# Kernel optimization log

Hardware: AMD Instinct MI355X
Metric: run time of the kernel (lower is better)

Reference implementation:

```python
import jax, jax.numpy as jnp
import numpy as np

N_PER_G = 100  # nodes per graph


def setup_inputs() -> dict:
    key = jax.random.key(0)
    ks = jax.random.split(key, 12)
    N, G, E = 100000, 1000, 1600000
    ninp, nout, K, H, H2 = 3, 10, 5, 64, 32
    x = jax.random.normal(ks[0], (N, ninp), jnp.float32)
    # within-graph random edges (contiguous node blocks per graph)
    epg = E // G
    gid = jnp.arange(E, dtype=jnp.int32) // epg
    src = jax.random.randint(ks[1], (E,), 0, N_PER_G, jnp.int32) + gid * N_PER_G
    dst = jax.random.randint(ks[2], (E,), 0, N_PER_G, jnp.int32) + gid * N_PER_G
    edge_index = jnp.stack([src, dst])
    batch = (jnp.arange(N, dtype=jnp.int32) // N_PER_G)
    lambda_max = 1.5 + 0.5 * jax.random.uniform(ks[3], (G,), jnp.float32)
    s = 0.05
    W1 = jax.random.normal(ks[4], (K, ninp, H), jnp.float32) * s
    b1 = jnp.zeros((H,), jnp.float32)
    W2 = jax.random.normal(ks[5], (K, H, H), jnp.float32) * s
    b2 = jnp.zeros((H,), jnp.float32)
    W3 = jax.random.normal(ks[6], (K, H, H), jnp.float32) * s
    b3 = jnp.zeros((H,), jnp.float32)
    bn_gamma = jnp.ones((H,), jnp.float32)
    bn_beta = jnp.zeros((H,), jnp.float32)
    bn_mean = jnp.zeros((H,), jnp.float32)
    bn_var = jnp.ones((H,), jnp.float32)
    fc1_w = jax.random.normal(ks[7], (H, H2), jnp.float32) * s
    fc1_b = jnp.zeros((H2,), jnp.float32)
    fc2_w = jax.random.normal(ks[8], (H2, nout), jnp.float32) * s
    fc2_b = jnp.zeros((nout,), jnp.float32)
    return dict(x=x, edge_index=edge_index, batch=batch, lambda_max=lambda_max,
                W1=W1, b1=b1, W2=W2, b2=b2, W3=W3, b3=b3,
                bn_gamma=bn_gamma, bn_beta=bn_beta, bn_mean=bn_mean, bn_var=bn_var,
                fc1_w=fc1_w, fc1_b=fc1_b, fc2_w=fc2_w, fc2_b=fc2_b)


def _cheb_conv(x, W, b, row, col, coef_edge, coef_loop):
    # PyG ChebConv with sym-normalized scaled Laplacian:
    # Lhat x = scatter_add(coef_edge * x[col] -> row) + coef_loop * x
    N = x.shape[0]
    def lhat(h):
        return jax.ops.segment_sum(coef_edge[:, None] * h[col], row,
                                   num_segments=N) + coef_loop[:, None] * h
    Tx0 = x
    out = Tx0 @ W[0]
    Tx1 = lhat(x)
    out = out + Tx1 @ W[1]
    for k in range(2, W.shape[0]):
        Tx2 = 2.0 * lhat(Tx1) - Tx0
        out = out + Tx2 @ W[k]
        Tx0, Tx1 = Tx1, Tx2
    return out + b


def reference(x, edge_index, batch, lambda_max,
              W1, b1, W2, b2, W3, b3,
              bn_gamma, bn_beta, bn_mean, bn_var,
              fc1_w, fc1_b, fc2_w, fc2_b):
    N = x.shape[0]
    G = lambda_max.shape[0]
    row, col = edge_index[0], edge_index[1]
    # sym Laplacian normalization, scaled by 2/lambda_max (per-graph)
    deg = jax.ops.segment_sum(jnp.ones_like(row, dtype=x.dtype), row, num_segments=N)
    dis = jnp.where(deg > 0, deg, 1.0) ** -0.5
    dis = jnp.where(deg > 0, dis, 0.0)
    lmax_e = lambda_max[batch[row]]
    coef_edge = -(2.0 / lmax_e) * dis[row] * dis[col]   # off-diagonal of Lhat
    coef_loop = 2.0 / lambda_max[batch] - 1.0           # diagonal of Lhat
    h = jax.nn.relu(_cheb_conv(x, W1, b1, row, col, coef_edge, coef_loop))
    h = jax.nn.relu(_cheb_conv(h, W2, b2, row, col, coef_edge, coef_loop))
    h = jax.nn.relu(_cheb_conv(h, W3, b3, row, col, coef_edge, coef_loop))
    # global mean pool over graphs
    sums = jax.ops.segment_sum(h, batch, num_segments=G)
    cnts = jax.ops.segment_sum(jnp.ones((N,), h.dtype), batch, num_segments=G)
    g = sums / jnp.maximum(cnts, 1.0)[:, None]
    # BatchNorm1d (eval mode, running stats), eps=1e-5
    g = (g - bn_mean) * jax.lax.rsqrt(bn_var + 1e-5) * bn_gamma + bn_beta
    g = jax.nn.relu(g @ fc1_w + fc1_b)
    return jax.nn.log_softmax(g @ fc2_w + fc2_b, axis=1)
```

## Files before the change

kernel.cpp:

```cpp
#include <hip/hip_runtime.h>

#define NPG 100
#define HF 64
#define NROW 128
#define SA 120
#define ST 72
#define CMW 28

typedef float  f4   __attribute__((ext_vector_type(4)));
typedef float  f16v __attribute__((ext_vector_type(16)));
typedef short  bf8  __attribute__((ext_vector_type(8)));

#define SZ_ARM (NROW * SA * 2)
#define SZ_T   (NROW * ST * 2)
#define OFF_ARM 0
#define OFF_T   SZ_ARM
#define OFF_CM  SZ_ARM
#define OFF_MISC (OFF_T + SZ_T)
#define SMEM_BYTES (OFF_MISC + 1280)

#define WT_TOTAL 46080

__device__ __forceinline__ unsigned short f2bf(float f) {
    unsigned u = __float_as_uint(f);
    u += 0x7fffu + ((u >> 16) & 1u);
    return (unsigned short)(u >> 16);
}
__device__ __forceinline__ float bf2f(unsigned short h) {
    return __uint_as_float(((unsigned)h) << 16);
}
__device__ __forceinline__ f16v zerov16() {
    f16v z;
    #pragma unroll
    for (int i = 0; i < 16; i++) z[i] = 0.f;
    return z;
}

__global__ void wconv(const float* __restrict__ W1, const float* __restrict__ W2,
                      const float* __restrict__ W3, unsigned short* __restrict__ ws)
{
    int idx = blockIdx.x * 256 + threadIdx.x;
    if (idx >= WT_TOTAL) return;
    float v;
    if (idx < 5120) {
        int k5 = idx >> 10, rem = idx & 1023, fo = rem >> 4, fi = rem & 15;
        v = (fi < 3) ? W1[(k5 * 3 + fi) * HF + fo] : 0.f;
    } else if (idx < 25600) {
        int j = idx - 5120;
        int k5 = j >> 12, rem = j & 4095, fo = rem >> 6, fi = rem & 63;
        v = W2[(k5 * HF + fi) * HF + fo];
    } else {
        int j = idx - 25600;
        int k5 = j >> 12, rem = j & 4095, fo = rem >> 6, fi = rem & 63;
        v = W3[(k5 * HF + fi) * HF + fo];
    }
    ws[idx] = f2bf(v);
}

__launch_bounds__(256, 2)
__global__ void cheb1b(const float* __restrict__ x, const int* __restrict__ ei,
                       const float* __restrict__ lambda_max,
                       const unsigned short* __restrict__ Wt,
                       const float* __restrict__ b1, const float* __restrict__ b2,
                       const float* __restrict__ b3,
                       const float* __restrict__ bng, const float* __restrict__ bnb,
                       const float* __restrict__ bnm, const float* __restrict__ bnv,
                       const float* __restrict__ fc1w, const float* __restrict__ fc1b,
                       const float* __restrict__ fc2w, const float* __restrict__ fc2b,
                       float* __restrict__ out, int E_total, int epg)
{
    extern __shared__ char sm[];
    const int tid = threadIdx.x;
    const int g = blockIdx.x;
    const int ebase = g * epg, nbase = g * NPG;
    const int wg = tid >> 6, lane = tid & 63;
    const int l31 = lane & 31, hh = lane >> 5;
    const int ht  = wg & 1;
    const int Mt0 = (wg >> 1) * 2;
    const int fo  = ht * 32 + l31;

    unsigned* Cm  = (unsigned*)(sm + OFF_CM);
    float* dis    = (float*)(sm + OFF_MISC);
    float* pool   = (float*)(sm + OFF_MISC + 448);
    float* gvn    = (float*)(sm + OFF_MISC + 704);
    float* zf     = (float*)(sm + OFF_MISC + 960);
    float* logits = (float*)(sm + OFF_MISC + 1088);
    float* lsep   = (float*)(sm + OFF_MISC + 1152);

    const float lam = lambda_max[g];
    const float two_l = 2.0f / lam;
    const float cl = two_l - 1.0f;

    for (int i = tid; i < (NROW * CMW) / 4; i += 256)
        ((f4*)Cm)[i] = (f4){0.f, 0.f, 0.f, 0.f};
    __syncthreads();
    for (int e = tid; e < epg; e += 256) {
        int r = ei[ebase + e] - nbase;
        int c = ei[E_total + ebase + e] - nbase;
        atomicAdd(&Cm[r * CMW + (c >> 2)], 1u << (8 * (c & 3)));
    }
    __syncthreads();
    if (tid < NPG) {
        unsigned s = 0;
        #pragma unroll
        for (int w = 0; w < CMW; w++) {
            unsigned u = Cm[tid * CMW + w];
            s += (u & 255) + ((u >> 8) & 255) + ((u >> 16) & 255) + (u >> 24);
        }
        dis[tid] = s > 0 ? rsqrtf((float)s) : 0.f;
    }
    __syncthreads();
    for (int u = tid; u < NROW * 56; u += 256) {
        int n = u / 56, p = (u % 56) * 2;
        float v0 = 0.f, v1 = 0.f;
        if (n < NPG) {
            unsigned w = Cm[n * CMW + (p >> 2)];
            int sh = 8 * (p & 3);
            float c0 = (float)((w >> sh) & 255);
            float c1 = (float)((w >> (sh + 8)) & 255);
            float base = -two_l * dis[n];
            v0 = (p     < NPG) ? c0 * base * dis[p]     : 0.f;
            v1 = (p + 1 < NPG) ? c1 * base * dis[p + 1] : 0.f;
            if (p == n)     v0 += cl;
            if (p + 1 == n) v1 += cl;
        }
        *(unsigned*)(sm + OFF_ARM + (n * SA + p) * 2) =
            (unsigned)f2bf(v0) | ((unsigned)f2bf(v1) << 16);
    }
    __syncthreads();

    for (int i = tid; i < SZ_T / 16; i += 256)
        ((f4*)(sm + OFF_T))[i] = (f4){0.f, 0.f, 0.f, 0.f};
    if (tid < HF) pool[tid] = 0.f;
    __syncthreads();
    if (tid < NPG) {
        unsigned short h0 = f2bf(x[(nbase + tid) * 3 + 0]);
        unsigned short h1 = f2bf(x[(nbase + tid) * 3 + 1]);
        unsigned short h2 = f2bf(x[(nbase + tid) * 3 + 2]);
        *(unsigned*)(sm + OFF_T + (tid * ST) * 2) = (unsigned)h0 | ((unsigned)h1 << 16);
        *(unsigned short*)(sm + OFF_T + (tid * ST + 2) * 2) = h2;
    }
    __syncthreads();

    f16v acc[2];
    unsigned prev[2][8], oldr[2][8];
    const float* bsv[3] = {b1, b2, b3};

    for (int L = 0; L < 3; L++) {
        const bool l1 = (L == 0);
        const unsigned short* Wl = l1 ? Wt : (Wt + (L == 1 ? 5120 : 25600));
        acc[0] = zerov16();
        acc[1] = zerov16();

        #pragma unroll
        for (int m = 0; m < 2; m++) {
            unsigned short tv[16];
            #pragma unroll
            for (int r = 0; r < 16; r++) {
                int np = (Mt0 + m) * 32 + (r & 3) + 8 * (r >> 2) + 4 * hh;
                tv[r] = *(const unsigned short*)(sm + OFF_T + (np * ST + fo) * 2);
            }
            #pragma unroll
            for (int p = 0; p < 8; p++)
                prev[m][p] = (unsigned)tv[2 * p] | ((unsigned)tv[2 * p + 1] << 16);
        }

        auto TW = [&](int k5) {
            const int nKs = l1 ? 1 : 4;
            for (int Ks = 0; Ks < nKs; Ks++) {
                bf8 bw;
                if (l1) bw = *(const bf8*)(Wl + (k5 * 64 + fo) * 16 + 8 * hh);
                else    bw = *(const bf8*)(Wl + (k5 * 64 + fo) * 64 + Ks * 16 + 8 * hh);
                #pragma unroll
                for (int m = 0; m < 2; m++) {
                    bf8 a = *(const bf8*)(sm + OFF_T +
                              (((Mt0 + m) * 32 + l31) * ST + Ks * 16 + 8 * hh) * 2);
                    acc[m] = __builtin_amdgcn_mfma_f32_32x32x16_bf16(a, bw, acc[m], 0, 0, 0);
                }
            }
        };

        TW(0);
        for (int s = 1; s <= 4; s++) {
            bf8 bfr[7];
            #pragma unroll
            for (int Ks = 0; Ks < 7; Ks++) {
                #pragma unroll
                for (int j = 0; j < 8; j++) {
                    int k = Ks * 16 + 8 * hh + j;
                    bfr[Ks][j] = *(const short*)(sm + OFF_T + (k * ST + fo) * 2);
                }
            }
            __syncthreads();
            #pragma unroll
            for (int m = 0; m < 2; m++) {
                f16v c = zerov16();
                #pragma unroll
                for (int Ks = 0; Ks < 7; Ks++) {
                    bf8 a = *(const bf8*)(sm + OFF_ARM +
                              (((Mt0 + m) * 32 + l31) * SA + Ks * 16 + 8 * hh) * 2);
                    c = __builtin_amdgcn_mfma_f32_32x32x16_bf16(a, bfr[Ks], c, 0, 0, 0);
                }
                unsigned short h[16];
                #pragma unroll
                for (int r = 0; r < 16; r++) {
                    float v = c[r];
                    if (s >= 2) {
                        unsigned short o = (unsigned short)
                            ((oldr[m][r >> 1] >> (16 * (r & 1))) & 0xffff);
                        v = 2.f * v - bf2f(o);
                    }
                    h[r] = f2bf(v);
                }
                #pragma unroll
                for (int p = 0; p < 8; p++) {
                    oldr[m][p] = prev[m][p];
                    prev[m][p] = (unsigned)h[2 * p] | ((unsigned)h[2 * p + 1] << 16);
                }
                #pragma unroll
                for (int r = 0; r < 16; r++) {
                    int np = (Mt0 + m) * 32 + (r & 3) + 8 * (r >> 2) + 4 * hh;
                    *(unsigned short*)(sm + OFF_T + (np * ST + fo) * 2) = h[r];
                }
            }
            __syncthreads();
            TW(s);
        }
        __syncthreads();

        const float bias = bsv[L][fo];
        if (L < 2) {
            #pragma unroll
            for (int m = 0; m < 2; m++) {
                #pragma unroll
                for (int r = 0; r < 16; r++) {
                    float h = fmaxf(acc[m][r] + bias, 0.f);
                    int np = (Mt0 + m) * 32 + (r & 3) + 8 * (r >> 2) + 4 * hh;
                    *(unsigned short*)(sm + OFF_T + (np * ST + fo) * 2) = f2bf(h);
                }
            }
            __syncthreads();
        } else {
            float ssum = 0.f;
            #pragma unroll
            for (int m = 0; m < 2; m++) {
                #pragma unroll
                for (int r = 0; r < 16; r++) {
                    int np = (Mt0 + m) * 32 + (r & 3) + 8 * (r >> 2) + 4 * hh;
                    float h = fmaxf(acc[m][r] + bias, 0.f);
                    if (np < NPG) ssum += h;
                }
            }
            ssum += __shfl_xor(ssum, 32, 64);
            if (hh == 0) atomicAdd(&pool[fo], ssum);
            __syncthreads();
        }
    }

    if (tid < HF) {
        float gv = pool[tid] * (1.0f / NPG);
        gv = (gv - bnm[tid]) * rsqrtf(bnv[tid] + 1e-5f) * bng[tid] + bnb[tid];
        gvn[tid] = gv;
    }
    __syncthreads();
    if (tid < 32) {
        float a = fc1b[tid];
        for (int f = 0; f < HF; f++) a += gvn[f] * fc1w[f * 32 + tid];
        zf[tid] = fmaxf(a, 0.f);
    }
    __syncthreads();
    if (tid < 10) {
        float a = fc2b[tid];
        for (int k = 0; k < 32; k++) a += zf[k] * fc2w[k * 10 + tid];
        logits[tid] = a;
    }
    __syncthreads();
    if (tid == 0) {
        float m = logits[0];
        for (int i = 1; i < 10; i++) m = fmaxf(m, logits[i]);
        float s = 0.f;
        for (int i = 0; i < 10; i++) s += expf(logits[i] - m);
        lsep[0] = m + logf(s);
    }
    __syncthreads();
    if (tid < 10) out[g * 10 + tid] = logits[tid] - lsep[0];
}

extern "C" void kernel_launch(void* const* d_in, const int* in_sizes, int n_in,
                              void* d_out, int out_size, void* d_ws, size_t ws_size,
                              hipStream_t stream) {
    const float* x    = (const float*)d_in[0];
    const int*   ei   = (const int*)d_in[1];
    const float* lmax = (const float*)d_in[3];
    const float* W1   = (const float*)d_in[4];
    const float* b1   = (const float*)d_in[5];
    const float* W2   = (const float*)d_in[6];
    const float* b2   = (const float*)d_in[7];
    const float* W3   = (const float*)d_in[8];
    const float* b3   = (const float*)d_in[9];
    const float* bng  = (const float*)d_in[10];
    const float* bnb  = (const float*)d_in[11];
    const float* bnm  = (const float*)d_in[12];
    const float* bnv  = (const float*)d_in[13];
    const float* fc1w = (const float*)d_in[14];
    const float* fc1b = (const float*)d_in[15];
    const float* fc2w = (const float*)d_in[16];
    const float* fc2b = (const float*)d_in[17];

    const int E = in_sizes[1] / 2;
    const int G = in_sizes[3];
    const int epg = E / G;

    unsigned short* Wt = (unsigned short*)d_ws;

    wconv<<<(WT_TOTAL + 255) / 256, 256, 0, stream>>>(W1, W2, W3, Wt);

    hipFuncSetAttribute((const void*)cheb1b,
                        hipFuncAttributeMaxDynamicSharedMemorySize, SMEM_BYTES);

    cheb1b<<<G, 256, SMEM_BYTES, stream>>>(x, ei, lmax, Wt, b1, b2, b3,
                                           bng, bnb, bnm, bnv, fc1w, fc1b, fc2w, fc2b,
                                           (float*)d_out, E, epg);
}
```

Measured before the change: 184.9 us.

## Keep Laplacian A-fragments in registers and add transposed T copy for vector loads

The scaled Laplacian tile is no longer materialised in shared memory. Each wave builds its bf16 MFMA A-fragments once, directly from the packed edge-count matrix, and keeps them in registers for all layers and Chebyshev steps. A second, feature-major (transposed) copy of the current T matrix is maintained in LDS, so the B operand of the Laplacian MFMA can be read with 16-byte vector loads instead of 56 scalar 2-byte loads. The cost is 56 extra VGPRs per thread for the fragments, extra packed stores on every step to keep both copies in sync, and a risk of spills under launch_bounds(256,2).

Result: faster. 172.0 us (-7.0%).

```diff
diff --git a/kernel.cpp b/kernel.cpp
--- a/kernel.cpp
+++ b/kernel.cpp
@@ -3,20 +3,20 @@
 #define NPG 100
 #define HF 64
 #define NROW 128
-#define SA 120
 #define ST 72
+#define SAT 136
 #define CMW 28
 
 typedef float  f4   __attribute__((ext_vector_type(4)));
 typedef float  f16v __attribute__((ext_vector_type(16)));
 typedef short  bf8  __attribute__((ext_vector_type(8)));
 
-#define SZ_ARM (NROW * SA * 2)
-#define SZ_T   (NROW * ST * 2)
-#define OFF_ARM 0
-#define OFF_T   SZ_ARM
-#define OFF_CM  SZ_ARM
-#define OFF_MISC (OFF_T + SZ_T)
+#define SZ_TC  (HF * SAT * 2)
+#define SZ_TRM (NROW * ST * 2)
+#define OFF_TC  0
+#define OFF_TRM SZ_TC
+#define OFF_CM  0
+#define OFF_MISC (OFF_TRM + SZ_TRM)
 #define SMEM_BYTES (OFF_MISC + 1280)
 
 #define WT_TOTAL 46080
@@ -58,16 +58,16 @@
 }
 
 __launch_bounds__(256, 2)
-__global__ void cheb1b(const float* __restrict__ x, const int* __restrict__ ei,
-                       const float* __restrict__ lambda_max,
-                       const unsigned short* __restrict__ Wt,
-                       const float* __restrict__ b1, const float* __restrict__ b2,
-                       const float* __restrict__ b3,
-                       const float* __restrict__ bng, const float* __restrict__ bnb,
-                       const float* __restrict__ bnm, const float* __restrict__ bnv,
-                       const float* __restrict__ fc1w, const float* __restrict__ fc1b,
-                       const float* __restrict__ fc2w, const float* __restrict__ fc2b,
-                       float* __restrict__ out, int E_total, int epg)
+__global__ void chebreg(const float* __restrict__ x, const int* __restrict__ ei,
+                        const float* __restrict__ lambda_max,
+                        const unsigned short* __restrict__ Wt,
+                        const float* __restrict__ b1, const float* __restrict__ b2,
+                        const float* __restrict__ b3,
+                        const float* __restrict__ bng, const float* __restrict__ bnb,
+                        const float* __restrict__ bnm, const float* __restrict__ bnv,
+                        const float* __restrict__ fc1w, const float* __restrict__ fc1b,
+                        const float* __restrict__ fc2w, const float* __restrict__ fc2b,
+                        float* __restrict__ out, int E_total, int epg)
 {
     extern __shared__ char sm[];
     const int tid = threadIdx.x;
@@ -100,45 +100,57 @@
         atomicAdd(&Cm[r * CMW + (c >> 2)], 1u << (8 * (c & 3)));
     }
     __syncthreads();
-    if (tid < NPG) {
-        unsigned s = 0;
+    if (tid < 112) {
+        float dv = 0.f;
+        if (tid < NPG) {
+            unsigned s = 0;
+            #pragma unroll
+            for (int w = 0; w < CMW; w++) {
+                unsigned u = Cm[tid * CMW + w];
+                s += (u & 255) + ((u >> 8) & 255) + ((u >> 16) & 255) + (u >> 24);
+            }
+            dv = s > 0 ? rsqrtf((float)s) : 0.f;
+        }
+        dis[tid] = dv;
+    }
+    __syncthreads();
+
+    bf8 af[2][7];
+    #pragma unroll
+    for (int m = 0; m < 2; m++) {
+        int rr = 32 * (Mt0 + m) + l31;
+        bool rv = (rr < NPG);
+        float base = rv ? (-two_l * dis[rr]) : 0.f;
         #pragma unroll
-        for (int w = 0; w < CMW; w++) {
-            unsigned u = Cm[tid * CMW + w];
-            s += (u & 255) + ((u >> 8) & 255) + ((u >> 16) & 255) + (u >> 24);
-        }
-        dis[tid] = s > 0 ? rsqrtf((float)s) : 0.f;
-    }
-    __syncthreads();
-    for (int u = tid; u < NROW * 56; u += 256) {
-        int n = u / 56, p = (u % 56) * 2;
-        float v0 = 0.f, v1 = 0.f;
-        if (n < NPG) {
-            unsigned w = Cm[n * CMW + (p >> 2)];
-            int sh = 8 * (p & 3);
-            float c0 = (float)((w >> sh) & 255);
-            float c1 = (float)((w >> (sh + 8)) & 255);
-            float base = -two_l * dis[n];
-            v0 = (p     < NPG) ? c0 * base * dis[p]     : 0.f;
-            v1 = (p + 1 < NPG) ? c1 * base * dis[p + 1] : 0.f;
-            if (p == n)     v0 += cl;
-            if (p + 1 == n) v1 += cl;
-        }
-        *(unsigned*)(sm + OFF_ARM + (n * SA + p) * 2) =
-            (unsigned)f2bf(v0) | ((unsigned)f2bf(v1) << 16);
-    }
-    __syncthreads();
-
-    for (int i = tid; i < SZ_T / 16; i += 256)
-        ((f4*)(sm + OFF_T))[i] = (f4){0.f, 0.f, 0.f, 0.f};
+        for (int Ks = 0; Ks < 7; Ks++) {
+            int k0 = Ks * 16 + 8 * hh;
+            unsigned w0 = rv ? Cm[rr * CMW + (k0 >> 2)]     : 0u;
+            unsigned w1 = rv ? Cm[rr * CMW + (k0 >> 2) + 1] : 0u;
+            #pragma unroll
+            for (int j = 0; j < 8; j++) {
+                int k = k0 + j;
+                unsigned cnt = (((j < 4) ? w0 : w1) >> (8 * (k & 3))) & 255u;
+                float v = base * (float)cnt * dis[k];
+                if (rv && k == rr) v += cl;
+                af[m][Ks][j] = (short)f2bf(v);
+            }
+        }
+    }
+    __syncthreads();
+
+    for (int i = tid; i < (SZ_TC + SZ_TRM) / 16; i += 256)
+        ((f4*)sm)[i] = (f4){0.f, 0.f, 0.f, 0.f};
     if (tid < HF) pool[tid] = 0.f;
     __syncthreads();
     if (tid < NPG) {
         unsigned short h0 = f2bf(x[(nbase + tid) * 3 + 0]);
         unsigned short h1 = f2bf(x[(nbase + tid) * 3 + 1]);
         unsigned short h2 = f2bf(x[(nbase + tid) * 3 + 2]);
-        *(unsigned*)(sm + OFF_T + (tid * ST) * 2) = (unsigned)h0 | ((unsigned)h1 << 16);
-        *(unsigned short*)(sm + OFF_T + (tid * ST + 2) * 2) = h2;
+        *(unsigned*)(sm + OFF_TRM + (tid * ST) * 2) = (unsigned)h0 | ((unsigned)h1 << 16);
+        *(unsigned short*)(sm + OFF_TRM + (tid * ST + 2) * 2) = h2;
+        *(unsigned short*)(sm + OFF_TC + (0 * SAT + tid) * 2) = h0;
+        *(unsigned short*)(sm + OFF_TC + (1 * SAT + tid) * 2) = h1;
+        *(unsigned short*)(sm + OFF_TC + (2 * SAT + tid) * 2) = h2;
     }
     __syncthreads();
 
@@ -158,7 +170,7 @@
             #pragma unroll
             for (int r = 0; r < 16; r++) {
                 int np = (Mt0 + m) * 32 + (r & 3) + 8 * (r >> 2) + 4 * hh;
-                tv[r] = *(const unsigned short*)(sm + OFF_T + (np * ST + fo) * 2);
+                tv[r] = *(const unsigned short*)(sm + OFF_TRM + (np * ST + fo) * 2);
             }
             #pragma unroll
             for (int p = 0; p < 8; p++)
@@ -173,7 +185,7 @@
                 else    bw = *(const bf8*)(Wl + (k5 * 64 + fo) * 64 + Ks * 16 + 8 * hh);
                 #pragma unroll
                 for (int m = 0; m < 2; m++) {
-                    bf8 a = *(const bf8*)(sm + OFF_T +
+                    bf8 a = *(const bf8*)(sm + OFF_TRM +
                               (((Mt0 + m) * 32 + l31) * ST + Ks * 16 + 8 * hh) * 2);
                     acc[m] = __builtin_amdgcn_mfma_f32_32x32x16_bf16(a, bw, acc[m], 0, 0, 0);
                 }
@@ -184,23 +196,16 @@
         for (int s = 1; s <= 4; s++) {
             bf8 bfr[7];
             #pragma unroll
-            for (int Ks = 0; Ks < 7; Ks++) {
-                #pragma unroll
-                for (int j = 0; j < 8; j++) {
-                    int k = Ks * 16 + 8 * hh + j;
-                    bfr[Ks][j] = *(const short*)(sm + OFF_T + (k * ST + fo) * 2);
-                }
-            }
+            for (int Ks = 0; Ks < 7; Ks++)
+                bfr[Ks] = *(const bf8*)(sm + OFF_TC +
+                            (fo * SAT + Ks * 16 + 8 * hh) * 2);
             __syncthreads();
             #pragma unroll
             for (int m = 0; m < 2; m++) {
                 f16v c = zerov16();
                 #pragma unroll
-                for (int Ks = 0; Ks < 7; Ks++) {
-                    bf8 a = *(const bf8*)(sm + OFF_ARM +
-                              (((Mt0 + m) * 32 + l31) * SA + Ks * 16 + 8 * hh) * 2);
-                    c = __builtin_amdgcn_mfma_f32_32x32x16_bf16(a, bfr[Ks], c, 0, 0, 0);
-                }
+                for (int Ks = 0; Ks < 7; Ks++)
+                    c = __builtin_amdgcn_mfma_f32_32x32x16_bf16(af[m][Ks], bfr[Ks], c, 0, 0, 0);
                 unsigned short h[16];
                 #pragma unroll
                 for (int r = 0; r < 16; r++) {
@@ -218,9 +223,17 @@
                     prev[m][p] = (unsigned)h[2 * p] | ((unsigned)h[2 * p + 1] << 16);
                 }
                 #pragma unroll
+                for (int q4 = 0; q4 < 4; q4++) {
+                    int np0 = (Mt0 + m) * 32 + 8 * q4 + 4 * hh;
+                    uint2 pk;
+                    pk.x = prev[m][2 * q4];
+                    pk.y = prev[m][2 * q4 + 1];
+                    *(uint2*)(sm + OFF_TC + (fo * SAT + np0) * 2) = pk;
+                }
+                #pragma unroll
                 for (int r = 0; r < 16; r++) {
                     int np = (Mt0 + m) * 32 + (r & 3) + 8 * (r >> 2) + 4 * hh;
-                    *(unsigned short*)(sm + OFF_T + (np * ST + fo) * 2) = h[r];
+                    *(unsigned short*)(sm + OFF_TRM + (np * ST + fo) * 2) = h[r];
                 }
             }
             __syncthreads();
@@ -232,11 +245,20 @@
         if (L < 2) {
             #pragma unroll
             for (int m = 0; m < 2; m++) {
+                unsigned short h[16];
                 #pragma unroll
                 for (int r = 0; r < 16; r++) {
-                    float h = fmaxf(acc[m][r] + bias, 0.f);
+                    h[r] = f2bf(fmaxf(acc[m][r] + bias, 0.f));
                     int np = (Mt0 + m) * 32 + (r & 3) + 8 * (r >> 2) + 4 * hh;
-                    *(unsigned short*)(sm + OFF_T + (np * ST + fo) * 2) = f2bf(h);
+                    *(unsigned short*)(sm + OFF_TRM + (np * ST + fo) * 2) = h[r];
+                }
+                #pragma unroll
+                for (int q4 = 0; q4 < 4; q4++) {
+                    int np0 = (Mt0 + m) * 32 + 8 * q4 + 4 * hh;
+                    uint2 pk;
+                    pk.x = (unsigned)h[4 * q4]     | ((unsigned)h[4 * q4 + 1] << 16);
+                    pk.y = (unsigned)h[4 * q4 + 2] | ((unsigned)h[4 * q4 + 3] << 16);
+                    *(uint2*)(sm + OFF_TC + (fo * SAT + np0) * 2) = pk;
                 }
             }
             __syncthreads();
@@ -315,10 +337,10 @@
 
     wconv<<<(WT_TOTAL + 255) / 256, 256, 0, stream>>>(W1, W2, W3, Wt);
 
-    hipFuncSetAttribute((const void*)cheb1b,
+    hipFuncSetAttribute((const void*)chebreg,
                         hipFuncAttributeMaxDynamicSharedMemorySize, SMEM_BYTES);
 
-    cheb1b<<<G, 256, SMEM_BYTES, stream>>>(x, ei, lmax, Wt, b1, b2, b3,
-                                           bng, bnb, bnm, bnv, fc1w, fc1b, fc2w, fc2b,
-                                           (float*)d_out, E, epg);
-}
+    chebreg<<<G, 256, SMEM_BYTES, stream>>>(x, ei, lmax, Wt, b1, b2, b3,
+                                            bng, bnb, bnm, bnv, fc1w, fc1b, fc2w, fc2b,
+                                            (float*)d_out, E, epg);
+}
```
